# Kernel tuning notes

Hardware: AMD Instinct MI355X
Metric: run time of the kernel (lower is better)

Reference implementation:

```python
import jax, jax.numpy as jnp
import numpy as np

B, C, N, L = 64, 32, 500, 12
C_OUT = 32
C_CAT = 9 * C  # (order*(support_len+1)+1)*c_in = 288


def setup_inputs() -> dict:
    key = jax.random.key(0)
    ks = jax.random.split(key, 7)
    x = jax.random.normal(ks[0], (B, C, N, L), dtype=jnp.float32)
    # row-stochastic-ish adjacencies: scale by 1/N to keep hops numerically tame
    A0 = jax.random.uniform(ks[1], (N, N), dtype=jnp.float32) / N
    A1 = jax.random.uniform(ks[2], (N, N), dtype=jnp.float32) / N
    A2 = jax.random.uniform(ks[3], (N, N), dtype=jnp.float32) / N
    A3 = jax.random.uniform(ks[4], (B, N, N), dtype=jnp.float32) / N
    W = jax.random.normal(ks[5], (C_OUT, C_CAT), dtype=jnp.float32) * 0.05
    b = jax.random.normal(ks[6], (C_OUT,), dtype=jnp.float32) * 0.05
    return {"x": x, "A0": A0, "A1": A1, "A2": A2, "A3": A3, "W": W, "b": b}


def reference(x, A0, A1, A2, A3, W, b):
    # x: [B, C, N, L]; A0..A2: [N, N]; A3: [B, N, N]; W: [C_OUT, 9*C]; b: [C_OUT]
    def hop2(h, A):  # static adjacency
        return jnp.einsum('ncvl,vw->ncwl', h, A)

    def hop3(h, A):  # batched (dynamic) adjacency
        return jnp.einsum('ncvl,nvw->ncwl', h, A)

    out = [x]
    for A in (A0, A1, A2):
        x1 = hop2(x, A)
        x2 = hop2(x1, A)
        out.extend([x1, x2])
    x1 = hop3(x, A3)
    x2 = hop3(x1, A3)
    out.extend([x1, x2])

    h = jnp.concatenate(out, axis=1)  # [B, 9C, N, L]
    # 1x1 Conv2d == channel mixing matmul + bias
    h = jnp.einsum('ncvl,oc->novl', h, W) + b[None, :, None, None]
    # dropout in eval mode: identity
    return h
```

## Files before the change

### kernel.cpp

```cpp
#include <hip/hip_runtime.h>

typedef unsigned short u16;
typedef __bf16 bf16x8 __attribute__((ext_vector_type(8)));
typedef float f32x4 __attribute__((ext_vector_type(4)));
typedef const unsigned int __attribute__((address_space(1))) gu32;
typedef unsigned int __attribute__((address_space(3))) lu32;

#define NN 500
#define LLc 12
#define CC 32
#define MM 384
#define KP 512
#define MT 96
#define NT2 128
#define XS_S 40
#define AS_S 40
#define CT2_S 136
#define TS_S 384
#define AT_ELS 256000

__device__ __forceinline__ u16 f2bf(float f) {
    union { float f; unsigned u; } cv; cv.f = f;
    unsigned u = cv.u;
    u += 0x7fffu + ((u >> 16) & 1u);
    return (u16)(u >> 16);
}
__device__ __forceinline__ float bf2f(u16 s) {
    union { unsigned u; float f; } cv; cv.u = ((unsigned)s) << 16;
    return cv.f;
}

__global__ __launch_bounds__(256) void atrans_all(
    const float* __restrict__ A0, const float* __restrict__ A1,
    const float* __restrict__ A2, const float* __restrict__ A3,
    u16* __restrict__ At_s, u16* __restrict__ At_b)
{
    __shared__ u16 Ls[32 * 36];
    const int t = threadIdx.x;
    const int n0 = blockIdx.x * 32;
    const int k0 = blockIdx.y * 32;
    const int z = blockIdx.z;
    const float* Ab; u16* Ob;
    if (z == 0)      { Ab = A0; Ob = At_s; }
    else if (z == 1) { Ab = A1; Ob = At_s + (long)AT_ELS; }
    else if (z == 2) { Ab = A2; Ob = At_s + 2L * AT_ELS; }
    else             { Ab = A3 + (long)(z - 3) * NN * NN; Ob = At_b + (long)(z - 3) * AT_ELS; }
    {
        int vl = t >> 3, u = t & 7;
        float4 v = make_float4(0.f, 0.f, 0.f, 0.f);
        if (k0 + vl < NN && n0 + 4 * u + 4 <= NN)
            v = *(const float4*)(Ab + (long)(k0 + vl) * NN + n0 + 4 * u);
        int nb = 4 * u;
        Ls[(nb + 0) * 36 + vl] = f2bf(v.x);
        Ls[(nb + 1) * 36 + vl] = f2bf(v.y);
        Ls[(nb + 2) * 36 + vl] = f2bf(v.z);
        Ls[(nb + 3) * 36 + vl] = f2bf(v.w);
    }
    __syncthreads();
    {
        int row = t >> 3, u = t & 7;
        if (n0 + row < NN)
            *(uint2*)(Ob + (long)(n0 + row) * KP + k0 + 4 * u) = *(const uint2*)(&Ls[row * 36 + 4 * u]);
    }
}

__global__ __launch_bounds__(256) void xpose_kernel(
    const float* __restrict__ x, u16* __restrict__ Xt)
{
    __shared__ u16 Ls[MM * 36];
    const int t = threadIdx.x;
    const int v0 = blockIdx.x * 32;
    const int b  = blockIdx.y;
    #pragma unroll
    for (int j = 0; j < 12; ++j) {
        int f = t + 256 * j;
        int c = f / 96;
        int r = f - c * 96;
        int vl = r / 3;
        int l3 = (r - vl * 3) * 4;
        float4 v = make_float4(0.f, 0.f, 0.f, 0.f);
        if (v0 + vl < NN)
            v = *(const float4*)(x + ((long)b * CC + c) * (NN * LLc) + (long)(v0 + vl) * LLc + l3);
        int mb = (c * LLc + l3) * 36 + vl;
        Ls[mb]       = f2bf(v.x);
        Ls[mb + 36]  = f2bf(v.y);
        Ls[mb + 72]  = f2bf(v.z);
        Ls[mb + 108] = f2bf(v.w);
    }
    __syncthreads();
    #pragma unroll
    for (int j = 0; j < 12; ++j) {
        int f = t + 256 * j;
        int row = f >> 3, u = f & 7;
        *(uint2*)(Xt + ((long)b * MM + row) * KP + v0 + 4 * u) = *(const uint2*)(&Ls[row * 36 + 4 * u]);
    }
}

__global__ __launch_bounds__(256) void wpack_kernel(
    const float* __restrict__ W, u16* __restrict__ Wp)
{
    const int t = threadIdx.x;
    #pragma unroll 1
    for (int k = 0; k < 72; ++k) {
        int idx = t + 256 * k;
        int j    = idx & 7;
        int lane = (idx >> 3) & 63;
        int p    = (idx >> 9) & 1;
        int mt   = (idx >> 10) & 1;
        int g    = idx >> 11;
        int o  = mt * 16 + (lane & 15);
        int kk = g * 32 + (lane >> 4) * 8 + j;
        float wv = W[o * 288 + kk];
        u16 hi = f2bf(wv);
        Wp[idx] = (p == 0) ? hi : f2bf(wv - bf2f(hi));
    }
}

__global__ __launch_bounds__(256, 3) void hop_fast3(
    const u16* __restrict__ Xsrc, long x_gstride, long x_bstride, int x_rstride, int x_klim,
    const u16* __restrict__ At_s,
    const u16* __restrict__ At_b,
    u16* __restrict__ Hout, long h_gstride)
{
    __shared__ __align__(16) u16 smem[13056];
    u16* As = smem;
    u16* Xs = smem + 5120;
    u16* Ct = smem;

    const int t = threadIdx.x;
    const int lane = t & 63;
    const int wv = t >> 6;
    const int f0 = blockIdx.x + 4 * blockIdx.y + 8 * blockIdx.z;
    const int w  = (f0 & 7) * 256 + (f0 >> 3);
    const int bx = w & 3;
    const int by = (w >> 2) & 1;
    const int zc = w >> 3;
    const int g  = zc & 3;
    const int b  = zc >> 2;
    const int n0 = bx * NT2;
    const int m0 = by * 192;
    const int ln = lane & 15;
    const int q8 = (lane >> 4) * 8;

    const u16* Ab = (g < 3) ? (At_s + (long)g * AT_ELS) : (At_b + (long)b * AT_ELS);
    const u16* Xb = Xsrc + (long)g * x_gstride + (long)b * x_bstride;
    u16* Ob = Hout + (long)g * h_gstride + (long)b * ((long)MM * NN);

    uint2 pa[4], px[6];
    auto loadA = [&](int k0) {
        #pragma unroll
        for (int j = 0; j < 4; ++j) {
            int f = t + 256 * j;
            int n = f >> 3, u = f & 7;
            uint2 v = make_uint2(0u, 0u);
            if (n0 + n < NN)
                v = *(const uint2*)(Ab + (long)(n0 + n) * KP + k0 + 4 * u);
            pa[j] = v;
        }
    };
    auto loadX = [&](int k0) {
        #pragma unroll
        for (int j = 0; j < 6; ++j) {
            int f = t + 256 * j;
            int r = f >> 3, u = f & 7;
            int k = k0 + 4 * u;
            uint2 v = make_uint2(0u, 0u);
            if (k < x_klim)
                v = *(const uint2*)(Xb + (long)(m0 + r) * x_rstride + k);
            px[j] = v;
        }
    };

    f32x4 acc[2][12];
    #pragma unroll
    for (int ns = 0; ns < 2; ++ns)
        #pragma unroll
        for (int i = 0; i < 12; ++i)
            #pragma unroll
            for (int r = 0; r < 4; ++r) acc[ns][i][r] = 0.f;

    loadA(0);
    loadX(0);
    #pragma unroll 1
    for (int s = 0; s < 16; ++s) {
        __syncthreads();
        #pragma unroll
        for (int j = 0; j < 4; ++j) {
            int f = t + 256 * j;
            *(uint2*)(&As[(f >> 3) * AS_S + 4 * (f & 7)]) = pa[j];
        }
        #pragma unroll
        for (int j = 0; j < 6; ++j) {
            int f = t + 256 * j;
            *(uint2*)(&Xs[(f >> 3) * XS_S + 4 * (f & 7)]) = px[j];
        }
        if (s < 15) {
            loadA(32 * (s + 1));
            loadX(32 * (s + 1));
        }
        __syncthreads();
        bf16x8 b0 = *(const bf16x8*)(&As[(wv * 32 + ln) * AS_S + q8]);
        bf16x8 b1 = *(const bf16x8*)(&As[(wv * 32 + 16 + ln) * AS_S + q8]);
        #pragma unroll
        for (int i = 0; i < 12; ++i) {
            bf16x8 af = *(const bf16x8*)(&Xs[(i * 16 + ln) * XS_S + q8]);
            acc[0][i] = __builtin_amdgcn_mfma_f32_16x16x32_bf16(af, b0, acc[0][i], 0, 0, 0);
            acc[1][i] = __builtin_amdgcn_mfma_f32_16x16x32_bf16(af, b1, acc[1][i], 0, 0, 0);
        }
    }

    #pragma unroll
    for (int h = 0; h < 2; ++h) {
        __syncthreads();
        #pragma unroll
        for (int ns = 0; ns < 2; ++ns) {
            int col = wv * 32 + ns * 16 + ln;
            #pragma unroll
            for (int i6 = 0; i6 < 6; ++i6) {
                int rb = i6 * 16 + (lane >> 4) * 4;
                #pragma unroll
                for (int r = 0; r < 4; ++r)
                    Ct[(rb + r) * CT2_S + col] = f2bf(acc[ns][h * 6 + i6][r]);
            }
        }
        __syncthreads();
        #pragma unroll
        for (int j = 0; j < 12; ++j) {
            int f = t + 256 * j;
            int row = f >> 5, u = f & 31;
            int n = n0 + 4 * u;
            if (n < NN)
                *(uint2*)(Ob + (long)(m0 + h * 96 + row) * NN + n) = *(const uint2*)(&Ct[row * CT2_S + 4 * u]);
        }
    }
}

__global__ __launch_bounds__(512, 4) void mix_mfma(
    const u16* __restrict__ Xt,
    const u16* __restrict__ H,
    const u16* __restrict__ Wp,
    const float* __restrict__ bias,
    float* __restrict__ out)
{
    __shared__ __align__(16) char smem[50176];
    u16*   Ls = (u16*)smem;
    float* Ct = (float*)smem;

    const int t   = threadIdx.x;
    const int wg  = blockIdx.y * 8 + blockIdx.x;
    const int swz = (wg & 7) * 64 + (wg >> 3);
    const int bx  = swz & 7;
    const int b   = swz >> 3;
    const int n0  = bx * 64;
    const int w    = t >> 6;
    const int lane = t & 63;
    const int kq   = lane >> 4;
    const int ln   = lane & 15;
    const int srow   = lane >> 3;
    const int schunk = (lane & 7) * 8;

    f32x4 acc[6][2];
    #pragma unroll
    for (int i = 0; i < 6; ++i)
        #pragma unroll
        for (int m = 0; m < 2; ++m)
            #pragma unroll
            for (int r = 0; r < 4; ++r) acc[i][m][r] = 0.f;

    #pragma unroll 1
    for (int g = 0; g < 9; ++g) {
        const u16* base; int rs;
        if (g == 0) { base = Xt + (long)b * (MM * KP); rs = KP; }
        else {
            int gg = g - 1;
            int buf = (gg & 1) ? 4 + (gg >> 1) : (gg >> 1);
            base = H + (long)buf * 12288000L + (long)b * 192000L; rs = NN;
        }
        __syncthreads();
        #pragma unroll
        for (int i = 0; i < 6; ++i) {
            int r0 = (w * 6 + i) * 8;
            const u16* src = base + (long)(r0 + srow) * rs + n0 + schunk;
            __builtin_amdgcn_global_load_lds((gu32*)src, (lu32*)(Ls + r0 * 64), 16, 0, 0);
        }
        asm volatile("s_waitcnt vmcnt(0)" ::: "memory");
        __syncthreads();
        uint4 wf[2][2];
        #pragma unroll
        for (int mt = 0; mt < 2; ++mt)
            #pragma unroll
            for (int p = 0; p < 2; ++p)
                wf[mt][p] = *(const uint4*)(Wp + ((((g * 2 + mt) * 2 + p) * 64 + lane) * 8));
        #pragma unroll
        for (int i = 0; i < 6; ++i) {
            int ct = w * 6 + i;
            int off0 = kq * 6144 + (ct >> 2) * 64 + (ct & 3) * 16 + ln;
            union { u16 s[8]; bf16x8 v; } fb;
            #pragma unroll
            for (int j = 0; j < 8; ++j) fb.s[j] = Ls[off0 + j * 768];
            #pragma unroll
            for (int mt = 0; mt < 2; ++mt) {
                acc[i][mt] = __builtin_amdgcn_mfma_f32_16x16x32_bf16(*(const bf16x8*)&wf[mt][0], fb.v, acc[i][mt], 0, 0, 0);
                acc[i][mt] = __builtin_amdgcn_mfma_f32_16x16x32_bf16(*(const bf16x8*)&wf[mt][1], fb.v, acc[i][mt], 0, 0, 0);
            }
        }
    }

    #pragma unroll
    for (int mt = 0; mt < 2; ++mt) {
        __syncthreads();
        #pragma unroll
        for (int i = 0; i < 6; ++i) {
            int col = (w * 6 + i) * 16 + ln;
            #pragma unroll
            for (int r = 0; r < 4; ++r)
                Ct[(kq * 4 + r) * 781 + col] = acc[i][mt][r];
        }
        __syncthreads();
        int o16 = t >> 5, u = t & 31;
        int og = mt * 16 + o16;
        float bs = bias[og];
        float* ob = out + (((long)b * CC + og) * NN + n0) * 12L;
        #pragma unroll
        for (int j2 = 0; j2 < 2; ++j2) {
            int n = u + 32 * j2;
            if (n0 + n < NN) {
                float v[12];
                #pragma unroll
                for (int l = 0; l < 12; ++l) v[l] = Ct[o16 * 781 + l * 64 + n] + bs;
                #pragma unroll
                for (int q = 0; q < 3; ++q)
                    *(float4*)(ob + (long)n * 12 + q * 4) = *(const float4*)&v[q * 4];
            }
        }
    }
}

__global__ __launch_bounds__(256, 3) void mix_all(
    const u16* __restrict__ Xt,
    const u16* __restrict__ H,
    const float* __restrict__ W,
    const float* __restrict__ bias,
    float* __restrict__ out)
{
    __shared__ __align__(16) float smem[96 * 36 + 288 * 33];
    float* ts = smem;
    float* Ws = smem + 96 * 36;

    const int t  = threadIdx.x;
    const int b  = blockIdx.y;
    const int w0 = blockIdx.x * 32;
    const int o  = t & 31;
    const int wq = t >> 5;
    const int w4 = wq * 4;
    const long HBUF = (long)64 * MM * NN;

    #pragma unroll
    for (int j = 0; j < 36; ++j) {
        int f = t + 256 * j;
        int oo = f & 31, ci = f >> 5;
        Ws[ci * 33 + oo] = W[oo * 288 + ci];
    }

    float acc[4][12];
    #pragma unroll
    for (int k = 0; k < 4; ++k)
        #pragma unroll
        for (int l = 0; l < 12; ++l) acc[k][l] = 0.f;

    uint2 px[3];
    auto loadq = [&](int q) {
        int g = q >> 2, c0 = (q & 3) << 3;
        const u16* base; int rs;
        if (g == 0) { base = Xt + (long)b * (MM * KP); rs = KP; }
        else {
            int gg = g - 1, i = gg >> 1;
            int buf = (gg & 1) ? 4 + i : i;
            base = H + (long)buf * HBUF + (long)b * ((long)MM * NN); rs = NN;
        }
        int m0c = c0 * 12;
        #pragma unroll
        for (int j = 0; j < 3; ++j) {
            int f = t + 256 * j;
            int r = f >> 3, u = f & 7;
            px[j] = *(const uint2*)(base + (long)(m0c + r) * rs + w0 + 4 * u);
        }
    };

    loadq(0);
    #pragma unroll 1
    for (int q = 0; q < 36; ++q) {
        __syncthreads();
        #pragma unroll
        for (int j = 0; j < 3; ++j) {
            int f = t + 256 * j;
            int r = f >> 3, u = f & 7;
            uint2 raw = px[j];
            float4 v = make_float4(bf2f((u16)(raw.x & 0xffffu)), bf2f((u16)(raw.x >> 16)),
                                   bf2f((u16)(raw.y & 0xffffu)), bf2f((u16)(raw.y >> 16)));
            *(float4*)(&ts[r * 36 + 4 * u]) = v;
        }
        if (q < 35) loadq(q + 1);
        __syncthreads();
        int g = q >> 2, c0 = (q & 3) << 3;
        #pragma unroll 1
        for (int cl = 0; cl < 8; ++cl) {
            float wgt = Ws[(g * 32 + c0 + cl) * 33 + o];
            #pragma unroll
            for (int l = 0; l < 12; ++l) {
                float4 h = *(const float4*)(&ts[(cl * 12 + l) * 36 + w4]);
                acc[0][l] += wgt * h.x;
                acc[1][l] += wgt * h.y;
                acc[2][l] += wgt * h.z;
                acc[3][l] += wgt * h.w;
            }
        }
    }

    #pragma unroll 1
    for (int r = 0; r < 4; ++r) {
        __syncthreads();
        if ((o >> 3) == r) {
            int ol = o & 7;
            #pragma unroll
            for (int k = 0; k < 4; ++k)
                #pragma unroll
                for (int l = 0; l < 12; ++l)
                    ts[ol * 388 + (w4 + k) * 12 + l] = acc[k][l];
        }
        __syncthreads();
        #pragma unroll
        for (int j = 0; j < 3; ++j) {
            int f4 = t + 256 * j;
            int ol = f4 / 96;
            int rem = f4 - ol * 96;
            int w  = rem / 3;
            int lq = rem - w * 3;
            if (w0 + w < NN) {
                float4 v = *(const float4*)(&ts[ol * 388 + w * 12 + lq * 4]);
                float bs = bias[r * 8 + ol];
                v.x += bs; v.y += bs; v.z += bs; v.w += bs;
                *(float4*)(out + (((long)b * CC + r * 8 + ol) * NN + w0 + w) * LLc + lq * 4) = v;
            }
        }
    }
}

__global__ __launch_bounds__(256, 4) void hop_fast(
    const u16* __restrict__ Xsrc, long x_bstride, int x_rstride, int x_klim,
    const u16* __restrict__ At,   long a_bstride,
    u16* __restrict__ hout)
{
    __shared__ __align__(16) u16 smem[13056];
    u16* As = smem;
    u16* Xs = smem + 5120;
    u16* Ct = smem;

    const int t = threadIdx.x;
    const int lane = t & 63;
    const int wv = t >> 6;
    const int n0 = blockIdx.x * NT2;
    const int m0 = blockIdx.y * MT;
    const int b  = blockIdx.z;
    const int ln = lane & 15;
    const int q8 = (lane >> 4) * 8;

    const u16* Ab = At + (long)b * a_bstride;
    const u16* Xb = Xsrc + (long)b * x_bstride;

    uint2 pa[4], px[3];
    auto loadA = [&](int k0) {
        #pragma unroll
        for (int j = 0; j < 4; ++j) {
            int f = t + 256 * j;
            int n = f >> 3, u = f & 7;
            uint2 v = make_uint2(0u, 0u);
            if (n0 + n < NN)
                v = *(const uint2*)(Ab + (long)(n0 + n) * KP + k0 + 4 * u);
            pa[j] = v;
        }
    };
    auto loadX = [&](int k0) {
        #pragma unroll
        for (int j = 0; j < 3; ++j) {
            int f = t + 256 * j;
            int r = f >> 3, u = f & 7;
            int k = k0 + 4 * u;
            uint2 v = make_uint2(0u, 0u);
            if (k < x_klim)
                v = *(const uint2*)(Xb + (long)(m0 + r) * x_rstride + k);
            px[j] = v;
        }
    };

    f32x4 acc[2][6];
    #pragma unroll
    for (int ns = 0; ns < 2; ++ns)
        #pragma unroll
        for (int i = 0; i < 6; ++i)
            #pragma unroll
            for (int r = 0; r < 4; ++r) acc[ns][i][r] = 0.f;

    loadA(0);
    loadX(0);
    #pragma unroll 1
    for (int s = 0; s < 16; ++s) {
        __syncthreads();
        #pragma unroll
        for (int j = 0; j < 4; ++j) {
            int f = t + 256 * j;
            *(uint2*)(&As[(f >> 3) * AS_S + 4 * (f & 7)]) = pa[j];
        }
        #pragma unroll
        for (int j = 0; j < 3; ++j) {
            int f = t + 256 * j;
            *(uint2*)(&Xs[(f >> 3) * XS_S + 4 * (f & 7)]) = px[j];
        }
        if (s < 15) {
            loadA(32 * (s + 1));
            loadX(32 * (s + 1));
        }
        __syncthreads();
        bf16x8 af[6];
        #pragma unroll
        for (int i = 0; i < 6; ++i)
            af[i] = *(const bf16x8*)(&Xs[(i * 16 + ln) * XS_S + q8]);
        #pragma unroll
        for (int ns = 0; ns < 2; ++ns) {
            bf16x8 bfr = *(const bf16x8*)(&As[(wv * 32 + ns * 16 + ln) * AS_S + q8]);
            #pragma unroll
            for (int i = 0; i < 6; ++i)
                acc[ns][i] = __builtin_amdgcn_mfma_f32_16x16x32_bf16(af[i], bfr, acc[ns][i], 0, 0, 0);
        }
    }

    __syncthreads();
    #pragma unroll
    for (int ns = 0; ns < 2; ++ns) {
        int col = wv * 32 + ns * 16 + ln;
        #pragma unroll
        for (int i = 0; i < 6; ++i) {
            int rb = i * 16 + (lane >> 4) * 4;
            #pragma unroll
            for (int r = 0; r < 4; ++r)
                Ct[(rb + r) * CT2_S + col] = f2bf(acc[ns][i][r]);
        }
    }
    __syncthreads();
    u16* Ob = hout + (long)b * ((long)MM * NN);
    #pragma unroll
    for (int j = 0; j < 12; ++j) {
        int f = t + 256 * j;
        int row = f >> 5, u = f & 31;
        int n = n0 + 4 * u;
        if (n < NN)
            *(uint2*)(Ob + (long)(m0 + row) * NN + n) = *(const uint2*)(&Ct[row * CT2_S + 4 * u]);
    }
}

__global__ __launch_bounds__(256, 2) void mix_kernel(
    const float* __restrict__ x,
    const u16* __restrict__ h1,
    const u16* __restrict__ h2,
    const float* __restrict__ W,
    const float* __restrict__ bias,
    int blk1, int blk2,
    float* __restrict__ out, int init)
{
    __shared__ __align__(16) float smem[CC * TS_S + 3 * 1056];
    float* ts = smem;
    float* Ws = smem + CC * TS_S;

    const int t = threadIdx.x;
    const int b = blockIdx.y;
    const int w0 = blockIdx.x * 32;
    const int o  = t & 15;
    const int wg = (t >> 4) & 7;
    const int lh = t >> 7;

    #pragma unroll
    for (int j = 0; j < 4; ++j) {
        int f = t + 256 * j;
        int oo = f & 31, c = f >> 5;
        Ws[c * 33 + oo]        = W[oo * 288 + blk1 * 32 + c];
        Ws[1056 + c * 33 + oo] = W[oo * 288 + blk2 * 32 + c];
        if (init) Ws[2112 + c * 33 + oo] = W[oo * 288 + c];
    }

    float acc2[2][4][6];
    #pragma unroll
    for (int a = 0; a < 2; ++a)
        #pragma unroll
        for (int q = 0; q < 4; ++q)
            #pragma unroll
            for (int l = 0; l < 6; ++l) acc2[a][q][l] = 0.f;

    auto stage_h = [&](const u16* h) {
        #pragma unroll
        for (int j = 0; j < 12; ++j) {
            int f = t + 256 * j;
            int row = f >> 3, u = f & 7;
            int w = w0 + 4 * u;
            uint2 raw = make_uint2(0u, 0u);
            if (w < NN)
                raw = *(const uint2*)(h + ((long)b * MM + row) * NN + w);
            int c = row / 12;
            int l = row - c * 12;
            float* dst = &ts[c * TS_S + l * 32 + 4 * u];
            dst[0] = bf2f((u16)(raw.x & 0xffffu));
            dst[1] = bf2f((u16)(raw.x >> 16));
            dst[2] = bf2f((u16)(raw.y & 0xffffu));
            dst[3] = bf2f((u16)(raw.y >> 16));
        }
    };
    auto accum = [&](const float* Wg) {
        for (int c = 0; c < CC; ++c) {
            float w1 = Wg[c * 33 + o];
            float w2 = Wg[c * 33 + o + 16];
            #pragma unroll
            for (int l6 = 0; l6 < 6; ++l6) {
                const float4 hv = *(const float4*)(&ts[c * TS_S + (lh * 6 + l6) * 32 + wg * 4]);
                acc2[0][0][l6] += w1 * hv.x;
                acc2[0][1][l6] += w1 * hv.y;
                acc2[0][2][l6] += w1 * hv.z;
                acc2[0][3][l6] += w1 * hv.w;
                acc2[1][0][l6] += w2 * hv.x;
                acc2[1][1][l6] += w2 * hv.y;
                acc2[1][2][l6] += w2 * hv.z;
                acc2[1][3][l6] += w2 * hv.w;
            }
        }
    };

    if (init) {
        #pragma unroll
        for (int j = 0; j < 12; ++j) {
            int f = t + 256 * j;
            int c = f / 96;
            int r = f - c * 96;
            int w = r / 3;
            int q = r - w * 3;
            float4 v = make_float4(0.f, 0.f, 0.f, 0.f);
            if (w0 + w < NN)
                v = *(const float4*)(x + ((long)b * CC + c) * (NN * LLc) + (long)(w0 + w) * LLc + q * 4);
            float* dst = &ts[c * TS_S + (q * 4) * 32 + w];
            dst[0]  = v.x; dst[32] = v.y; dst[64] = v.z; dst[96] = v.w;
        }
        __syncthreads();
        accum(Ws + 2112);
        __syncthreads();
    }
    stage_h(h1);
    __syncthreads();
    accum(Ws);
    __syncthreads();
    stage_h(h2);
    __syncthreads();
    accum(Ws + 1056);

    #pragma unroll
    for (int oh = 0; oh < 2; ++oh) {
        int oo = o + 16 * oh;
        float bs = init ? bias[oo] : 0.f;
        #pragma unroll
        for (int q = 0; q < 4; ++q) {
            int w = w0 + wg * 4 + q;
            if (w < NN) {
                float* op = out + ((long)b * CC + oo) * (NN * LLc) + (long)w * LLc + lh * 6;
                #pragma unroll
                for (int p = 0; p < 3; ++p) {
                    float2* pp = (float2*)op + p;
                    float2 v;
                    if (init) {
                        v.x = bs + acc2[oh][q][2 * p];
                        v.y = bs + acc2[oh][q][2 * p + 1];
                    } else {
                        v = *pp;
                        v.x += acc2[oh][q][2 * p];
                        v.y += acc2[oh][q][2 * p + 1];
                    }
                    *pp = v;
                }
            }
        }
    }
}

extern "C" void kernel_launch(void* const* d_in, const int* in_sizes, int n_in,
                              void* d_out, int out_size, void* d_ws, size_t ws_size,
                              hipStream_t stream) {
    const float* x    = (const float*)d_in[0];
    const float* A0   = (const float*)d_in[1];
    const float* A1   = (const float*)d_in[2];
    const float* A2   = (const float*)d_in[3];
    const float* A3   = (const float*)d_in[4];
    const float* W    = (const float*)d_in[5];
    const float* bias = (const float*)d_in[6];
    float* out = (float*)d_out;
    char* ws = (char*)d_ws;

    const size_t HBUF_ELS  = (size_t)64 * MM * NN;
    const size_t H8_BYTES  = 8 * HBUF_ELS * 2;
    const size_t AT_BYTES  = (size_t)AT_ELS * 2;
    const size_t A3T_BYTES = 64 * AT_BYTES;
    const size_t XT_BYTES  = (size_t)64 * MM * KP * 2;
    const size_t need2 = H8_BYTES + 3 * AT_BYTES + A3T_BYTES + XT_BYTES;
    const size_t WPK_BYTES = 36864;
    const size_t need3 = need2 + WPK_BYTES;

    dim3 blk(256);
    dim3 hgrid(4, 2, 256);

    if (ws_size >= need3) {
        u16* Hb   = (u16*)ws;
        u16* At_s = (u16*)(ws + H8_BYTES);
        u16* A3t  = At_s + 3L * AT_ELS;
        u16* Xt   = (u16*)(ws + H8_BYTES + 3 * AT_BYTES + A3T_BYTES);
        u16* Wpk  = (u16*)(ws + need2);

        atrans_all<<<dim3(16, 16, 67), blk, 0, stream>>>(A0, A1, A2, A3, At_s, A3t);
        xpose_kernel<<<dim3(16, 64), blk, 0, stream>>>(x, Xt);
        wpack_kernel<<<dim3(1), blk, 0, stream>>>(W, Wpk);
        hop_fast3<<<hgrid, blk, 0, stream>>>(
            Xt, 0L, (long)MM * KP, KP, KP, At_s, A3t, Hb, (long)HBUF_ELS);
        hop_fast3<<<hgrid, blk, 0, stream>>>(
            Hb, (long)HBUF_ELS, (long)MM * NN, NN, NN, At_s, A3t,
            Hb + 4 * HBUF_ELS, (long)HBUF_ELS);
        mix_mfma<<<dim3(8, 64), dim3(512), 0, stream>>>(Xt, Hb, Wpk, bias, out);
        return;
    }

    if (ws_size >= need2) {
        u16* H    = (u16*)ws;
        u16* At_s = (u16*)(ws + H8_BYTES);
        u16* A3t  = At_s + 3L * AT_ELS;
        u16* Xt   = (u16*)(ws + H8_BYTES + 3 * AT_BYTES + A3T_BYTES);

        atrans_all<<<dim3(16, 16, 67), blk, 0, stream>>>(A0, A1, A2, A3, At_s, A3t);
        xpose_kernel<<<dim3(16, 64), blk, 0, stream>>>(x, Xt);
        hop_fast3<<<hgrid, blk, 0, stream>>>(
            Xt, 0L, (long)MM * KP, KP, KP, At_s, A3t, H, (long)HBUF_ELS);
        hop_fast3<<<hgrid, blk, 0, stream>>>(
            H, (long)HBUF_ELS, (long)MM * NN, NN, NN, At_s, A3t,
            H + 4 * HBUF_ELS, (long)HBUF_ELS);
        mix_all<<<dim3(16, 64), blk, 0, stream>>>(Xt, H, W, bias, out);
        return;
    }

    const size_t H_BYTES   = HBUF_ELS * 2;
    const size_t need_at   = 2 * H_BYTES + 3 * AT_BYTES + A3T_BYTES;
    const size_t need_full = need_at + XT_BYTES;

    u16* H1 = (u16*)ws;
    u16* H2 = (u16*)(ws + H_BYTES);
    u16* At0 = (u16*)(ws + 2 * H_BYTES);
    u16* A3t = At0 + 3L * AT_ELS;
    u16* Xt  = (u16*)(ws + need_at);
    (void)need_full;

    dim3 fgrid(4, 4, 64);
    dim3 mgrid(16, 64);

    xpose_kernel<<<dim3(16, 64), blk, 0, stream>>>(x, Xt);
    atrans_all<<<dim3(16, 16, 67), blk, 0, stream>>>(A0, A1, A2, A3, At0, A3t);

    const long XT_BS = (long)MM * KP;
    const long H_BS  = (long)MM * NN;
    u16* Atp[4] = {At0, At0 + (long)AT_ELS, At0 + 2L * AT_ELS, A3t};

    for (int i = 0; i < 4; ++i) {
        long a_bs = (i == 3) ? (long)AT_ELS : 0;
        hop_fast<<<fgrid, blk, 0, stream>>>(Xt, XT_BS, KP, KP, Atp[i], a_bs, H1);
        hop_fast<<<fgrid, blk, 0, stream>>>(H1, H_BS, NN, NN, Atp[i], a_bs, H2);
        mix_kernel<<<mgrid, blk, 0, stream>>>(i == 0 ? x : nullptr, H1, H2, W, bias,
                                              2 * i + 1, 2 * i + 2, out, i == 0 ? 1 : 0);
    }
}
```

Measured before the change: 394.1 us.

## Add double-buffered hop kernel with padded K-stride hop buffers

Adds hop_fast4, which double-buffers the adjacency and activation tiles in shared memory with async global-to-LDS loads, so the next K-slice loads while MFMAs run on the current one. It also uses XOR-swizzled LDS addressing. Hop outputs are stored with a padded row stride of 512, zero-filled past N, so the second hop can read them like the transposed input without bounds handling; mix_mfma now takes the strides as parameters. This costs more workspace and more LDS per block, which may reduce occupancy, and it writes extra padding bytes.

Result: faster. 370.8 us (-5.9%).

```diff
diff --git a/kernel.cpp b/kernel.cpp
--- a/kernel.cpp
+++ b/kernel.cpp
@@ -116,6 +116,111 @@
     }
 }
 
+__global__ __launch_bounds__(256, 3) void hop_fast4(
+    const u16* __restrict__ Xsrc, long x_gstride, long x_bstride,
+    const u16* __restrict__ At_s,
+    const u16* __restrict__ At_b,
+    u16* __restrict__ Hout, long h_gstride)
+{
+    __shared__ __align__(16) u16 smem[20480];
+    u16* Ct = smem;
+
+    const int t = threadIdx.x;
+    const int lane = t & 63;
+    const int wv = t >> 6;
+    const int f0 = blockIdx.x + 4 * blockIdx.y + 8 * blockIdx.z;
+    const int w  = (f0 & 7) * 256 + (f0 >> 3);
+    const int bx = w & 3;
+    const int by = (w >> 2) & 1;
+    const int zc = w >> 3;
+    const int g  = zc & 3;
+    const int b  = zc >> 2;
+    const int n0 = bx * NT2;
+    const int m0 = by * 192;
+    const int ln  = lane & 15;
+    const int q16 = lane >> 4;
+
+    const u16* Ab = (g < 3) ? (At_s + (long)g * AT_ELS) : (At_b + (long)b * AT_ELS);
+    const u16* Xb = Xsrc + (long)g * x_gstride + (long)b * x_bstride;
+    u16* Ob = Hout + (long)g * h_gstride + (long)b * ((long)MM * KP);
+
+    const int rbase = lane >> 2;
+    const int coff  = (((lane & 3) ^ ((lane >> 3) & 3)) << 3);
+    const int rsel  = ((q16 ^ ((ln >> 1) & 3)) << 3);
+
+    auto STAGE = [&](int kk, int pb) {
+        #pragma unroll
+        for (int j = 0; j < 5; ++j) {
+            int o = (wv * 5 + j) << 10;
+            const u16* src;
+            if (o < 8192) {
+                src = Ab + (long)(n0 + (o >> 6) + rbase) * KP + kk + coff;
+            } else {
+                src = Xb + (long)(m0 + (o >> 6) - 128 + rbase) * KP + kk + coff;
+            }
+            __builtin_amdgcn_global_load_lds((gu32*)src,
+                (lu32*)((char*)smem + pb * 20480 + o), 16, 0, 0);
+        }
+    };
+
+    f32x4 acc[2][12];
+    #pragma unroll
+    for (int ns = 0; ns < 2; ++ns)
+        #pragma unroll
+        for (int i = 0; i < 12; ++i)
+            #pragma unroll
+            for (int r = 0; r < 4; ++r) acc[ns][i][r] = 0.f;
+
+    STAGE(0, 0);
+    asm volatile("s_waitcnt vmcnt(0)" ::: "memory");
+    __syncthreads();
+
+    #pragma unroll 1
+    for (int s = 0; s < 16; ++s) {
+        const int pb = s & 1;
+        if (s < 15) STAGE(32 * (s + 1), pb ^ 1);
+        const u16* As = smem + pb * 10240;
+        const u16* Xs = As + 4096;
+        const int rowA0 = wv * 32 + ln;
+        bf16x8 b0 = *(const bf16x8*)(&As[rowA0 * 32 + rsel]);
+        bf16x8 b1 = *(const bf16x8*)(&As[(rowA0 + 16) * 32 + rsel]);
+        #pragma unroll
+        for (int i = 0; i < 12; ++i) {
+            bf16x8 af = *(const bf16x8*)(&Xs[(i * 16 + ln) * 32 + rsel]);
+            acc[0][i] = __builtin_amdgcn_mfma_f32_16x16x32_bf16(af, b0, acc[0][i], 0, 0, 0);
+            acc[1][i] = __builtin_amdgcn_mfma_f32_16x16x32_bf16(af, b1, acc[1][i], 0, 0, 0);
+        }
+        asm volatile("s_waitcnt vmcnt(0)" ::: "memory");
+        __syncthreads();
+    }
+
+    #pragma unroll
+    for (int h = 0; h < 2; ++h) {
+        __syncthreads();
+        #pragma unroll
+        for (int ns = 0; ns < 2; ++ns) {
+            int col = wv * 32 + ns * 16 + ln;
+            #pragma unroll
+            for (int i6 = 0; i6 < 6; ++i6) {
+                int rb = i6 * 16 + (lane >> 4) * 4;
+                #pragma unroll
+                for (int r = 0; r < 4; ++r)
+                    Ct[(rb + r) * CT2_S + col] = f2bf(acc[ns][h * 6 + i6][r]);
+            }
+        }
+        __syncthreads();
+        #pragma unroll
+        for (int j = 0; j < 12; ++j) {
+            int f = t + 256 * j;
+            int row = f >> 5, u = f & 31;
+            int n = n0 + 4 * u;
+            uint2 v = make_uint2(0u, 0u);
+            if (n < NN) v = *(const uint2*)(&Ct[row * CT2_S + 4 * u]);
+            *(uint2*)(Ob + (long)(m0 + h * 96 + row) * KP + n) = v;
+        }
+    }
+}
+
 __global__ __launch_bounds__(256, 3) void hop_fast3(
     const u16* __restrict__ Xsrc, long x_gstride, long x_bstride, int x_rstride, int x_klim,
     const u16* __restrict__ At_s,
@@ -240,7 +345,8 @@
     const u16* __restrict__ H,
     const u16* __restrict__ Wp,
     const float* __restrict__ bias,
-    float* __restrict__ out)
+    float* __restrict__ out,
+    long h_gs, long h_bs, int h_rs)
 {
     __shared__ __align__(16) char smem[50176];
     u16*   Ls = (u16*)smem;
@@ -274,7 +380,7 @@
         else {
             int gg = g - 1;
             int buf = (gg & 1) ? 4 + (gg >> 1) : (gg >> 1);
-            base = H + (long)buf * 12288000L + (long)b * 192000L; rs = NN;
+            base = H + (long)buf * h_gs + (long)b * h_bs; rs = h_rs;
         }
         __syncthreads();
         #pragma unroll
@@ -707,9 +813,32 @@
     const size_t need2 = H8_BYTES + 3 * AT_BYTES + A3T_BYTES + XT_BYTES;
     const size_t WPK_BYTES = 36864;
     const size_t need3 = need2 + WPK_BYTES;
+    const size_t HB2_ELS  = (size_t)64 * MM * KP;
+    const size_t H8B_PAD  = 8 * HB2_ELS * 2;
+    const size_t need4 = H8B_PAD + 3 * AT_BYTES + A3T_BYTES + XT_BYTES + WPK_BYTES;
 
     dim3 blk(256);
     dim3 hgrid(4, 2, 256);
+
+    if (ws_size >= need4) {
+        u16* Hb   = (u16*)ws;
+        u16* At_s = (u16*)(ws + H8B_PAD);
+        u16* A3t  = At_s + 3L * AT_ELS;
+        u16* Xt   = (u16*)(ws + H8B_PAD + 3 * AT_BYTES + A3T_BYTES);
+        u16* Wpk  = Xt + (size_t)64 * MM * KP;
+
+        atrans_all<<<dim3(16, 16, 67), blk, 0, stream>>>(A0, A1, A2, A3, At_s, A3t);
+        xpose_kernel<<<dim3(16, 64), blk, 0, stream>>>(x, Xt);
+        wpack_kernel<<<dim3(1), blk, 0, stream>>>(W, Wpk);
+        hop_fast4<<<hgrid, blk, 0, stream>>>(
+            Xt, 0L, (long)MM * KP, At_s, A3t, Hb, (long)HB2_ELS);
+        hop_fast4<<<hgrid, blk, 0, stream>>>(
+            Hb, (long)HB2_ELS, (long)MM * KP, At_s, A3t,
+            Hb + 4 * HB2_ELS, (long)HB2_ELS);
+        mix_mfma<<<dim3(8, 64), dim3(512), 0, stream>>>(
+            Xt, Hb, Wpk, bias, out, (long)HB2_ELS, (long)MM * KP, KP);
+        return;
+    }
 
     if (ws_size >= need3) {
         u16* Hb   = (u16*)ws;
@@ -726,7 +855,8 @@
         hop_fast3<<<hgrid, blk, 0, stream>>>(
             Hb, (long)HBUF_ELS, (long)MM * NN, NN, NN, At_s, A3t,
             Hb + 4 * HBUF_ELS, (long)HBUF_ELS);
-        mix_mfma<<<dim3(8, 64), dim3(512), 0, stream>>>(Xt, Hb, Wpk, bias, out);
+        mix_mfma<<<dim3(8, 64), dim3(512), 0, stream>>>(
+            Xt, Hb, Wpk, bias, out, (long)HBUF_ELS, (long)MM * NN, NN);
         return;
     }
 
@@ -749,14 +879,12 @@
 
     const size_t H_BYTES   = HBUF_ELS * 2;
     const size_t need_at   = 2 * H_BYTES + 3 * AT_BYTES + A3T_BYTES;
-    const size_t need_full = need_at + XT_BYTES;
 
     u16* H1 = (u16*)ws;
     u16* H2 = (u16*)(ws + H_BYTES);
     u16* At0 = (u16*)(ws + 2 * H_BYTES);
     u16* A3t = At0 + 3L * AT_ELS;
     u16* Xt  = (u16*)(ws + need_at);
-    (void)need_full;
 
     dim3 fgrid(4, 4, 64);
     dim3 mgrid(16, 64);
```
